# Kernel optimization log

Hardware: AMD Instinct MI355X
Metric: run time of the kernel (lower is better)

The kernel has to match this reference:

```python
import jax, jax.numpy as jnp
import numpy as np
from jax import lax

B, T, D_IN, D_CB, K_CB, H_MID = 32, 512, 1024, 256, 8192, 512

def setup_inputs() -> dict:
    key = jax.random.key(0)
    ks = jax.random.split(key, 12)
    s = 0.02
    return {
        "x": jax.random.normal(ks[0], (B, T, D_IN), jnp.float32),
        "w1": jax.random.normal(ks[1], (H_MID, D_IN), jnp.float32) * s,
        "b1": jnp.zeros((H_MID,), jnp.float32),
        "w2": jax.random.normal(ks[2], (D_CB, H_MID), jnp.float32) * s,
        "b2": jnp.zeros((D_CB,), jnp.float32),
        "conv_w": jax.random.normal(ks[3], (D_CB, D_CB, 3), jnp.float32) * s,
        "conv_b": jnp.zeros((D_CB,), jnp.float32),
        "codebook": jax.random.uniform(ks[4], (K_CB, D_CB), jnp.float32, -1.0 / K_CB, 1.0 / K_CB),
        "gru_wih": jax.random.normal(ks[5], (3 * D_CB, D_CB), jnp.float32) * s,
        "gru_whh": jax.random.normal(ks[6], (3 * D_CB, D_CB), jnp.float32) * s,
        "gru_bih": jnp.zeros((3 * D_CB,), jnp.float32),
        "gru_bhh": jnp.zeros((3 * D_CB,), jnp.float32),
    }

def _forward(x, w1, b1, w2, b2, conv_w, conv_b, codebook, gru_wih, gru_whh, gru_bih, gru_bhh):
    # feature_processor (dropout is identity at eval): [B,T,D_IN] -> [B,T,D_CB]
    h = jax.nn.relu(jnp.einsum('btd,hd->bth', x, w1) + b1)
    h = jax.nn.relu(jnp.einsum('bth,ch->btc', h, w2) + b2)
    # temporal conv1d, kernel 3, pad 1 (T > 1 here)
    f = jnp.transpose(h, (0, 2, 1))  # NCT
    f = lax.conv_general_dilated(f, conv_w, (1,), 'SAME', dimension_numbers=('NCH', 'OIH', 'NCH'))
    f = f + conv_b[None, :, None]
    features = jnp.transpose(f, (0, 2, 1))  # [B,T,D_CB]
    # quantize: squared-Euclidean nearest codebook entry (same argmin as cdist)
    flat = features.reshape(-1, features.shape[-1])  # [B*T, D_CB]
    d2 = (jnp.sum(flat * flat, axis=1, keepdims=True)
          - 2.0 * (flat @ codebook.T)
          + jnp.sum(codebook * codebook, axis=1))  # [B*T, K]
    idx = jnp.argmin(d2, axis=-1)
    quantized = codebook[idx].reshape(features.shape)  # [B,T,D_CB]
    token_indices = idx.reshape(features.shape[0], features.shape[1])
    commitment_loss = jnp.mean((features - lax.stop_gradient(quantized)) ** 2)
    codebook_loss = jnp.mean((quantized - lax.stop_gradient(features)) ** 2)
    # context predictor: 1-layer GRU over quantized[:, :-1]
    q_in = quantized[:, :-1]  # [B,T-1,D_CB]
    xproj = jnp.einsum('btd,hd->bth', q_in, gru_wih) + gru_bih  # [B,T-1,3H]
    Hd = quantized.shape[-1]
    def step(hprev, xt):
        gh = hprev @ gru_whh.T + gru_bhh  # [B,3H]
        xr, xz, xn = xt[:, :Hd], xt[:, Hd:2 * Hd], xt[:, 2 * Hd:]
        hr, hz, hn = gh[:, :Hd], gh[:, Hd:2 * Hd], gh[:, 2 * Hd:]
        r = jax.nn.sigmoid(xr + hr)
        z = jax.nn.sigmoid(xz + hz)
        n = jnp.tanh(xn + r * hn)
        hnew = (1.0 - z) * n + z * hprev
        return hnew, hnew
    h0 = jnp.zeros((q_in.shape[0], Hd), q_in.dtype)
    _, hs = lax.scan(step, h0, jnp.transpose(xproj, (1, 0, 2)))
    context = jnp.transpose(hs, (1, 0, 2))  # [B,T-1,D_CB]
    context_loss = jnp.mean((context - features[:, 1:]) ** 2)
    vq_loss = commitment_loss + 0.25 * codebook_loss + 0.1 * context_loss
    return token_indices, quantized, commitment_loss, codebook_loss, context_loss, vq_loss

def reference(x, w1, b1, w2, b2, conv_w, conv_b, codebook, gru_wih, gru_whh, gru_bih, gru_bhh):
    return _forward(x, w1, b1, w2, b2, conv_w, conv_b, codebook, gru_wih, gru_whh, gru_bih, gru_bhh)
```

## Files before the change

### kernel.cpp

```cpp
#include <hip/hip_runtime.h>
#include <math.h>

#define NB 32
#define NT 512
#define NDIN 1024
#define NDCB 256
#define NKCB 8192
#define NHMID 512
#define NROWS (NB*NT)

typedef _Float16 half2_t __attribute__((ext_vector_type(2)));
typedef _Float16 f16x8 __attribute__((ext_vector_type(8)));
typedef __attribute__((ext_vector_type(8))) short bf16x8;
typedef __attribute__((ext_vector_type(8))) unsigned short u16x8;
typedef __attribute__((ext_vector_type(4))) float f32x4;

__device__ __forceinline__ unsigned short f2bf(float x) {
    unsigned int u = __float_as_uint(x);
    return (unsigned short)((u + 0x7fffu + ((u >> 16) & 1u)) >> 16);
}

#if __has_builtin(__builtin_amdgcn_fdot2)
__device__ __forceinline__ float dot2f(half2_t a, half2_t b, float c) {
    return __builtin_amdgcn_fdot2(a, b, c, false);
}
#else
__device__ __forceinline__ float dot2f(half2_t a, half2_t b, float c) {
    return fmaf((float)a[0], (float)b[0], fmaf((float)a[1], (float)b[1], c));
}
#endif

template<bool RELU>
__global__ __launch_bounds__(256) void gemm_nt_f64_kernel(
    const float* __restrict__ A, const float* __restrict__ Bm,
    const float* __restrict__ bias, float* __restrict__ C,
    int M, int N, int K)
{
    __shared__ double a_s[16*64];
    __shared__ double b_s[16*64];
    const int tid = threadIdx.x;
    const int bn0 = blockIdx.x * 64;
    const int bm0 = blockIdx.y * 64;
    const int lr = tid >> 2;
    const int kq = (tid & 3) << 2;
    const int tx = tid & 15, ty = tid >> 4;
    double acc[4][4] = {};
    const float* Ap = A + (size_t)(bm0 + lr) * K + kq;
    const float* Bp = Bm + (size_t)(bn0 + lr) * K + kq;
    for (int kt = 0; kt < K; kt += 16) {
        float4 a = *(const float4*)(Ap + kt);
        float4 b = *(const float4*)(Bp + kt);
        __syncthreads();
        a_s[(kq+0)*64+lr] = (double)a.x; a_s[(kq+1)*64+lr] = (double)a.y;
        a_s[(kq+2)*64+lr] = (double)a.z; a_s[(kq+3)*64+lr] = (double)a.w;
        b_s[(kq+0)*64+lr] = (double)b.x; b_s[(kq+1)*64+lr] = (double)b.y;
        b_s[(kq+2)*64+lr] = (double)b.z; b_s[(kq+3)*64+lr] = (double)b.w;
        __syncthreads();
        #pragma unroll
        for (int kk = 0; kk < 16; kk++) {
            double aa[4], bb[4];
            #pragma unroll
            for (int u = 0; u < 4; u++) { aa[u] = a_s[kk*64 + ty*4 + u]; bb[u] = b_s[kk*64 + tx*4 + u]; }
            #pragma unroll
            for (int i = 0; i < 4; i++)
                #pragma unroll
                for (int j = 0; j < 4; j++)
                    acc[i][j] = fma(aa[i], bb[j], acc[i][j]);
        }
    }
    const float4 b4 = *(const float4*)&bias[bn0 + tx*4];
    const double bc[4] = {(double)b4.x, (double)b4.y, (double)b4.z, (double)b4.w};
    #pragma unroll
    for (int i = 0; i < 4; i++) {
        float o[4];
        #pragma unroll
        for (int j = 0; j < 4; j++) {
            double v = acc[i][j] + bc[j];
            if (RELU) v = fmax(v, 0.0);
            o[j] = (float)v;
        }
        *(float4*)&C[(size_t)(bm0 + ty*4 + i)*N + bn0 + tx*4] =
            make_float4(o[0], o[1], o[2], o[3]);
    }
}

__global__ __launch_bounds__(256) void conv3_f64_kernel(
    const float* __restrict__ H2, const float* __restrict__ W3,
    const float* __restrict__ bias, float* __restrict__ F)
{
    __shared__ double a_s[16*68];
    __shared__ double b_s[3][16*64];
    const int tid = threadIdx.x;
    const int bn0 = blockIdx.x * 64;
    const int bm0 = blockIdx.y * 64;
    const int lr = tid >> 2;
    const int kq = (tid & 3) << 2;
    const int tx = tid & 15, ty = tid >> 4;
    const int tmod = bm0 & (NT-1);
    const bool has_top = (tmod != 0);
    const bool has_bot = (tmod + 64 < NT);
    double acc[4][4] = {};
    for (int kt = 0; kt < NDCB; kt += 16) {
        float4 a = make_float4(0.f,0.f,0.f,0.f);
        if (lr >= 1 || has_top)
            a = *(const float4*)&H2[(size_t)(bm0 - 1 + lr)*NDCB + kt + kq];
        float4 e = make_float4(0.f,0.f,0.f,0.f);
        int l2 = 0, kq2 = 0;
        if (tid < 8) {
            l2 = 64 + (tid >> 2); kq2 = (tid & 3) << 2;
            if (l2 == 64 || has_bot)
                e = *(const float4*)&H2[(size_t)(bm0 - 1 + l2)*NDCB + kt + kq2];
        }
        float4 w[3];
        #pragma unroll
        for (int s = 0; s < 3; s++)
            w[s] = *(const float4*)&W3[(size_t)s*65536 + (size_t)(bn0 + lr)*NDCB + kt + kq];
        __syncthreads();
        a_s[(kq+0)*68+lr]=(double)a.x; a_s[(kq+1)*68+lr]=(double)a.y;
        a_s[(kq+2)*68+lr]=(double)a.z; a_s[(kq+3)*68+lr]=(double)a.w;
        if (tid < 8) {
            a_s[(kq2+0)*68+l2]=(double)e.x; a_s[(kq2+1)*68+l2]=(double)e.y;
            a_s[(kq2+2)*68+l2]=(double)e.z; a_s[(kq2+3)*68+l2]=(double)e.w;
        }
        #pragma unroll
        for (int s = 0; s < 3; s++) {
            b_s[s][(kq+0)*64+lr]=(double)w[s].x; b_s[s][(kq+1)*64+lr]=(double)w[s].y;
            b_s[s][(kq+2)*64+lr]=(double)w[s].z; b_s[s][(kq+3)*64+lr]=(double)w[s].w;
        }
        __syncthreads();
        #pragma unroll
        for (int kk = 0; kk < 16; kk++) {
            double aa[6];
            #pragma unroll
            for (int u = 0; u < 6; u++) aa[u] = a_s[kk*68 + ty*4 + u];
            #pragma unroll
            for (int s = 0; s < 3; s++) {
                double bb[4];
                #pragma unroll
                for (int u = 0; u < 4; u++) bb[u] = b_s[s][kk*64 + tx*4 + u];
                #pragma unroll
                for (int i = 0; i < 4; i++)
                    #pragma unroll
                    for (int j = 0; j < 4; j++)
                        acc[i][j] = fma(aa[i+s], bb[j], acc[i][j]);
            }
        }
    }
    const float4 b4 = *(const float4*)&bias[bn0 + tx*4];
    const double bc[4] = {(double)b4.x, (double)b4.y, (double)b4.z, (double)b4.w};
    #pragma unroll
    for (int i = 0; i < 4; i++) {
        const size_t base = (size_t)(bm0 + ty*4 + i)*NDCB + bn0 + tx*4;
        *(float4*)&F[base] = make_float4((float)(acc[i][0]+bc[0]), (float)(acc[i][1]+bc[1]),
                                         (float)(acc[i][2]+bc[2]), (float)(acc[i][3]+bc[3]));
    }
}

__global__ __launch_bounds__(512) void vq_kernel(
    const float* __restrict__ F, const float* __restrict__ CB,
    const unsigned short* __restrict__ CBH,
    const float* __restrict__ cnorm, float* __restrict__ idx_out,
    float* __restrict__ qout, float* __restrict__ msd_acc)
{
    __shared__ unsigned short a_bf[64*256];
    __shared__ unsigned short b_bf[128*256];
    __shared__ float cn_s[128];
    __shared__ float red_v[64*64];
    __shared__ int   red_i[64*64];
    __shared__ int   bests[64];
    __shared__ int   cand[64][12];
    __shared__ int   ccnt[64];
    const int tid = threadIdx.x;
    const int m0 = blockIdx.x * 64;

    #pragma unroll
    for (int u = 0; u < 4; u++) {
        int e = tid + u*512;
        int row = e >> 5, c = e & 31;
        const float* src = &F[(size_t)(m0+row)*NDCB + c*8];
        float4 f0 = *(const float4*)src;
        float4 f1 = *(const float4*)(src+4);
        u16x8 p;
        p[0]=f2bf(f0.x); p[1]=f2bf(f0.y); p[2]=f2bf(f0.z); p[3]=f2bf(f0.w);
        p[4]=f2bf(f1.x); p[5]=f2bf(f1.y); p[6]=f2bf(f1.z); p[7]=f2bf(f1.w);
        *(u16x8*)((char*)a_bf + row*512 + ((c*16) ^ ((row&7)<<4))) = p;
    }

    const int w = tid >> 6, lane = tid & 63;
    const int l15 = lane & 15, kg = lane >> 4;
    const int rbase = (w & 3) << 4, cbase = (w >> 2) << 6;
    const char* aP = (const char*)a_bf + (size_t)(rbase + l15)*512;
    const char* bP = (const char*)b_bf + (size_t)(cbase + l15)*512;
    const int swz = (lane & 7) << 4;

    float mv1[4], mv2[4]; int mi1[4], mi2[4];
    #pragma unroll
    for (int i = 0; i < 4; i++) { mv1[i]=3.0e38f; mv2[i]=3.0e38f; mi1[i]=0x7fffffff; mi2[i]=0x7fffffff; }

    for (int n0 = 0; n0 < NKCB; n0 += 128) {
        __syncthreads();
        #pragma unroll
        for (int u = 0; u < 8; u++) {
            int e = tid + u*512;
            int row = e >> 5, c = e & 31;
            u16x8 v = *(const u16x8*)&CBH[(size_t)(n0+row)*NDCB + c*8];
            *(u16x8*)((char*)b_bf + row*512 + ((c*16) ^ ((row&7)<<4))) = v;
        }
        if (tid < 128) cn_s[tid] = cnorm[n0 + tid];
        __syncthreads();
        f32x4 acc[4] = {{0.f,0.f,0.f,0.f},{0.f,0.f,0.f,0.f},{0.f,0.f,0.f,0.f},{0.f,0.f,0.f,0.f}};
        #pragma unroll
        for (int kt = 0; kt < 8; kt++) {
            const int ko = (kt*64 + kg*16) ^ swz;
            bf16x8 av = *(const bf16x8*)(aP + ko);
            #pragma unroll
            for (int f = 0; f < 4; f++) {
                bf16x8 bv = *(const bf16x8*)(bP + f*8192 + ko);
                acc[f] = __builtin_amdgcn_mfma_f32_16x16x32_bf16(av, bv, acc[f], 0, 0, 0);
            }
        }
        #pragma unroll
        for (int f = 0; f < 4; f++) {
            const int col = n0 + cbase + f*16 + l15;
            const float cnv = cn_s[cbase + f*16 + l15];
            #pragma unroll
            for (int i = 0; i < 4; i++) {
                float s = fmaf(-2.0f, acc[f][i], cnv);
                if (s < mv1[i]) { mv2[i]=mv1[i]; mi2[i]=mi1[i]; mv1[i]=s; mi1[i]=col; }
                else if (s < mv2[i]) { mv2[i]=s; mi2[i]=col; }
            }
        }
    }
    #pragma unroll
    for (int i = 0; i < 4; i++) {
        const int row = rbase + kg*4 + i;
        const int eb  = (w>>2)*32 + l15*2;
        red_v[row*64 + eb]   = mv1[i]; red_i[row*64 + eb]   = mi1[i];
        red_v[row*64 + eb+1] = mv2[i]; red_i[row*64 + eb+1] = mi2[i];
    }
    __syncthreads();
    if (tid < 64) {
        float bv = 3.0e38f; int bi = 0x7fffffff;
        for (int e = 0; e < 64; e++) {
            float v = red_v[tid*64 + e]; int ii = red_i[tid*64 + e];
            if (v < bv || (v == bv && ii < bi)) { bv = v; bi = ii; }
        }
        int cnt = 0;
        for (int e = 0; e < 64; e++) {
            if (red_v[tid*64 + e] < bv + 1.0e-5f) {
                if (cnt < 12) cand[tid][cnt] = red_i[tid*64 + e];
                cnt++;
            }
        }
        bests[tid] = bi;
        ccnt[tid] = (cnt > 12) ? 12 : cnt;
    }
    __syncthreads();
    {
        const int wid = tid >> 6, lane2 = tid & 63;
        for (int r = wid; r < 64; r += 8) {
            const int nc = ccnt[r];
            if (nc < 2) continue;
            double sf = 0.0;
            #pragma unroll
            for (int u = 0; u < 4; u++) {
                double fv = (double)F[(size_t)(m0+r)*NDCB + lane2*4 + u];
                sf = fma(fv, fv, sf);
            }
            #pragma unroll
            for (int off = 32; off > 0; off >>= 1) sf += __shfl_down(sf, off);
            const float sf32 = (float)sf;
            float bd2 = 0.0f; int bidx = 0x7fffffff;
            for (int c = 0; c < nc; c++) {
                const int k = cand[r][c];
                double g = 0.0;
                #pragma unroll
                for (int u = 0; u < 4; u++) {
                    double cv = (double)CB[(size_t)k*NDCB + lane2*4 + u];
                    double fv = (double)F[(size_t)(m0+r)*NDCB + lane2*4 + u];
                    g = fma(cv, fv, g);
                }
                #pragma unroll
                for (int off = 32; off > 0; off >>= 1) g += __shfl_down(g, off);
                if (lane2 == 0) {
                    const float G32 = (float)g;
                    const float t  = sf32 - 2.0f*G32;
                    const float d2 = t + cnorm[k];
                    if (c == 0 || d2 < bd2 || (d2 == bd2 && k < bidx)) { bd2 = d2; bidx = k; }
                }
            }
            if (lane2 == 0) bests[r] = bidx;
        }
    }
    __syncthreads();
    if (tid < 64) idx_out[m0 + tid] = (float)bests[tid];
    float lsum = 0.0f;
    #pragma unroll
    for (int s = 0; s < 8; s++) {
        int e = tid + s*512;
        int row = e >> 6, kqe = (e & 63) << 2;
        float4 q = *(const float4*)&CB[(size_t)bests[row]*NDCB + kqe];
        float4 f = *(const float4*)&F[(size_t)(m0+row)*NDCB + kqe];
        float dx=f.x-q.x, dy=f.y-q.y, dz=f.z-q.z, dw=f.w-q.w;
        lsum += dx*dx + dy*dy + dz*dz + dw*dw;
        *(float4*)&qout[(size_t)(m0+row)*NDCB + kqe] = q;
    }
    red_v[tid] = lsum;
    __syncthreads();
    for (int off = 256; off > 0; off >>= 1) {
        if (tid < off) red_v[tid] += red_v[tid + off];
        __syncthreads();
    }
    if (tid == 0) atomicAdd(msd_acc, red_v[0]);
}

__global__ __launch_bounds__(512) void xproj_mfma_kernel(
    const float* __restrict__ Q, const unsigned short* __restrict__ WIHH,
    const float* __restrict__ bias, float* __restrict__ C)
{
    __shared__ unsigned short a_h[64*256];
    __shared__ unsigned short b_h[128*256];
    const int tid = threadIdx.x;
    const int m0 = blockIdx.x * 64;

    #pragma unroll
    for (int u = 0; u < 4; u++) {
        int e = tid + u*512;
        int row = e >> 5, c = e & 31;
        const float* src = &Q[(size_t)(m0+row)*NDCB + c*8];
        float4 f0 = *(const float4*)src;
        float4 f1 = *(const float4*)(src+4);
        f16x8 p;
        p[0]=(_Float16)(f0.x*8192.0f); p[1]=(_Float16)(f0.y*8192.0f);
        p[2]=(_Float16)(f0.z*8192.0f); p[3]=(_Float16)(f0.w*8192.0f);
        p[4]=(_Float16)(f1.x*8192.0f); p[5]=(_Float16)(f1.y*8192.0f);
        p[6]=(_Float16)(f1.z*8192.0f); p[7]=(_Float16)(f1.w*8192.0f);
        *(f16x8*)((char*)a_h + row*512 + ((c*16) ^ ((row&7)<<4))) = p;
    }

    const int w = tid >> 6, lane = tid & 63;
    const int l15 = lane & 15, kg = lane >> 4;
    const int rbase = (w & 3) << 4, cbase = (w >> 2) << 6;
    const char* aP = (const char*)a_h + (size_t)(rbase + l15)*512;
    const char* bP = (const char*)b_h + (size_t)(cbase + l15)*512;
    const int swz = (lane & 7) << 4;

    for (int n0 = 0; n0 < 768; n0 += 128) {
        __syncthreads();
        #pragma unroll
        for (int u = 0; u < 8; u++) {
            int e = tid + u*512;
            int row = e >> 5, c = e & 31;
            u16x8 v = *(const u16x8*)&WIHH[(size_t)(n0+row)*NDCB + c*8];
            *(u16x8*)((char*)b_h + row*512 + ((c*16) ^ ((row&7)<<4))) = v;
        }
        __syncthreads();
        f32x4 acc[4] = {{0.f,0.f,0.f,0.f},{0.f,0.f,0.f,0.f},{0.f,0.f,0.f,0.f},{0.f,0.f,0.f,0.f}};
        #pragma unroll
        for (int kt = 0; kt < 8; kt++) {
            const int ko = (kt*64 + kg*16) ^ swz;
            f16x8 av = *(const f16x8*)(aP + ko);
            #pragma unroll
            for (int f = 0; f < 4; f++) {
                f16x8 bv = *(const f16x8*)(bP + f*8192 + ko);
                acc[f] = __builtin_amdgcn_mfma_f32_16x16x32_f16(av, bv, acc[f], 0, 0, 0);
            }
        }
        #pragma unroll
        for (int f = 0; f < 4; f++) {
            const int col = n0 + cbase + f*16 + l15;
            const float bv = bias[col];
            #pragma unroll
            for (int i = 0; i < 4; i++) {
                const int row = m0 + rbase + kg*4 + i;
                C[(size_t)row*768 + col] = fmaf(acc[f][i], 1.0f/8192.0f, bv);
            }
        }
    }
}

__device__ __forceinline__ void gru_body(
    const float* __restrict__ XP, const float* __restrict__ WHH,
    const float* __restrict__ bhh, const float* __restrict__ F,
    float* __restrict__ ctx_acc)
{
    __shared__ float part[3][2][256];
    __shared__ uint4 hpk[2][32];
    __shared__ float red[256];
    const int tid = threadIdx.x;
    const int b = blockIdx.x;
    const int j = tid & 255;
    const int q = tid >> 8;
    half2_t wr[64], wz[64], wn[64];
    {
        const float* rp = WHH + (size_t)j*256 + q*128;
        #pragma unroll
        for (int k = 0; k < 32; k++) {
            float4 vr = *(const float4*)(rp + 4*k);
            float4 vz = *(const float4*)(rp + 65536 + 4*k);
            float4 vn = *(const float4*)(rp + 131072 + 4*k);
            wr[2*k+0] = (half2_t){(_Float16)vr.x, (_Float16)vr.y};
            wr[2*k+1] = (half2_t){(_Float16)vr.z, (_Float16)vr.w};
            wz[2*k+0] = (half2_t){(_Float16)vz.x, (_Float16)vz.y};
            wz[2*k+1] = (half2_t){(_Float16)vz.z, (_Float16)vz.w};
            wn[2*k+0] = (half2_t){(_Float16)vn.x, (_Float16)vn.y};
            wn[2*k+1] = (half2_t){(_Float16)vn.z, (_Float16)vn.w};
        }
    }
    if (tid < 64) hpk[tid >> 5][tid & 31] = make_uint4(0u, 0u, 0u, 0u);
    const float bb0 = bhh[j], bb1 = bhh[256+j], bb2 = bhh[512+j];
    const float* xpb = XP + (size_t)b*NT*768;
    const float* fb  = F  + (size_t)b*NT*NDCB;
    float hprev = 0.0f, lsum = 0.0f;
    __syncthreads();
    int cur = 0;
    for (int t = 0; t < NT-1; t++) {
        float xr = 0.f, xz = 0.f, xn = 0.f, fv = 0.f;
        if (tid < 256) {
            const float* xp = xpb + (size_t)t*768;
            xr = xp[j]; xz = xp[256+j]; xn = xp[512+j];
            fv = fb[(size_t)(t+1)*NDCB + j];
        }
        float a0=0.f, c0=0.f, a1=0.f, c1=0.f, a2=0.f, c2=0.f;
        #pragma unroll
        for (int kk = 0; kk < 16; kk++) {
            uint4 hp = hpk[cur][q*16 + kk];
            half2_t h0 = __builtin_bit_cast(half2_t, hp.x);
            half2_t h1 = __builtin_bit_cast(half2_t, hp.y);
            half2_t h2 = __builtin_bit_cast(half2_t, hp.z);
            half2_t h3 = __builtin_bit_cast(half2_t, hp.w);
            a0 = dot2f(wr[4*kk+0], h0, a0); c0 = dot2f(wr[4*kk+1], h1, c0);
            a1 = dot2f(wz[4*kk+0], h0, a1); c1 = dot2f(wz[4*kk+1], h1, c1);
            a2 = dot2f(wn[4*kk+0], h0, a2); c2 = dot2f(wn[4*kk+1], h1, c2);
            a0 = dot2f(wr[4*kk+2], h2, a0); c0 = dot2f(wr[4*kk+3], h3, c0);
            a1 = dot2f(wz[4*kk+2], h2, a1); c1 = dot2f(wz[4*kk+3], h3, c1);
            a2 = dot2f(wn[4*kk+2], h2, a2); c2 = dot2f(wn[4*kk+3], h3, c2);
        }
        part[0][q][j] = a0 + c0; part[1][q][j] = a1 + c1; part[2][q][j] = a2 + c2;
        __syncthreads();
        if (tid < 256) {
            float ghr = part[0][0][j] + part[0][1][j] + bb0;
            float ghz = part[1][0][j] + part[1][1][j] + bb1;
            float ghn = part[2][0][j] + part[2][1][j] + bb2;
            float r = 1.0f/(1.0f + __expf(-(xr + ghr)));
            float z = 1.0f/(1.0f + __expf(-(xz + ghz)));
            float v = fmaf(r, ghn, xn);
            v = fminf(fmaxf(v, -12.0f), 12.0f);
            float ev = __expf(-2.0f*v);
            float n = (1.0f - ev)/(1.0f + ev);
            float hnew = (1.0f - z)*n + z*hprev;
            float d = hnew - fv;
            lsum = fmaf(d, d, lsum);
            float nb = __shfl_down(hnew, 1);
            if (!(j & 1)) {
                half2_t p; p[0] = (_Float16)hnew; p[1] = (_Float16)nb;
                ((unsigned int*)&hpk[cur ^ 1][0])[j >> 1] = __builtin_bit_cast(unsigned int, p);
            }
            hprev = hnew;
        }
        __syncthreads();
        cur ^= 1;
    }
    if (tid < 256) red[j] = lsum;
    __syncthreads();
    for (int off = 128; off > 0; off >>= 1) {
        if (tid < off) red[tid] += red[tid + off];
        __syncthreads();
    }
    if (tid == 0) atomicAdd(ctx_acc, red[0]);
}

__global__ __attribute__((amdgpu_flat_work_group_size(512, 512), amdgpu_waves_per_eu(2, 2)))
void gru_a(const float* __restrict__ XP, const float* __restrict__ WHH,
           const float* __restrict__ bhh, const float* __restrict__ F,
           float* __restrict__ ctx_acc)
{ gru_body(XP, WHH, bhh, F, ctx_acc); }

__global__ __launch_bounds__(512, 2)
void gru_b(const float* __restrict__ XP, const float* __restrict__ WHH,
           const float* __restrict__ bhh, const float* __restrict__ F,
           float* __restrict__ ctx_acc)
{ gru_body(XP, WHH, bhh, F, ctx_acc); }

__global__ __launch_bounds__(512)
void gru_c(const float* __restrict__ XP, const float* __restrict__ WHH,
           const float* __restrict__ bhh, const float* __restrict__ F,
           float* __restrict__ ctx_acc)
{ gru_body(XP, WHH, bhh, F, ctx_acc); }

__global__ __launch_bounds__(256) void prep_kernel(
    const float* __restrict__ conv_w, float* __restrict__ w3,
    const float* __restrict__ wih, unsigned short* __restrict__ wihh,
    float* __restrict__ accv)
{
    int e = blockIdx.x*256 + threadIdx.x;
    if (e == 0) { accv[0] = 0.0f; accv[1] = 0.0f; }
    {
        int k = e >> 16;
        int r = e & 65535;
        int c = r >> 8, i = r & 255;
        w3[e] = conv_w[(size_t)c*768 + i*3 + k];
    }
    {
        _Float16 h = (_Float16)wih[e];
        wihh[e] = __builtin_bit_cast(unsigned short, h);
    }
}

__global__ __launch_bounds__(256) void cb2bf_kernel(
    const float* __restrict__ cb, unsigned short* __restrict__ cbh)
{
    int e = (blockIdx.x*256 + threadIdx.x) * 4;
    float4 v = *(const float4*)&cb[e];
    unsigned short p0 = f2bf(v.x), p1 = f2bf(v.y), p2 = f2bf(v.z), p3 = f2bf(v.w);
    unsigned long long pk = (unsigned long long)p0 | ((unsigned long long)p1 << 16)
                          | ((unsigned long long)p2 << 32) | ((unsigned long long)p3 << 48);
    *(unsigned long long*)&cbh[e] = pk;
}

__global__ __launch_bounds__(64) void cnorm_kernel(
    const float* __restrict__ CB, float* __restrict__ cn)
{
    const int k = blockIdx.x;
    const int lane = threadIdx.x;
    float4 v = *(const float4*)&CB[(size_t)k*NDCB + lane*4];
    double s = (double)v.x*(double)v.x + (double)v.y*(double)v.y
             + (double)v.z*(double)v.z + (double)v.w*(double)v.w;
    #pragma unroll
    for (int off = 32; off > 0; off >>= 1) s += __shfl_down(s, off);
    if (lane == 0) cn[k] = (float)s;
}

__global__ void finalize_kernel(const float* __restrict__ acc, float* __restrict__ out)
{
    if (threadIdx.x == 0) {
        float msd = acc[0] * (1.0f/4194304.0f);
        float ctx = acc[1] * (1.0f/4184064.0f);
        out[0] = msd;
        out[1] = msd;
        out[2] = ctx;
        out[3] = 1.25f*msd + 0.1f*ctx;
    }
}

extern "C" void kernel_launch(void* const* d_in, const int* in_sizes, int n_in,
                              void* d_out, int out_size, void* d_ws, size_t ws_size,
                              hipStream_t stream) {
    const float* x      = (const float*)d_in[0];
    const float* w1     = (const float*)d_in[1];
    const float* b1     = (const float*)d_in[2];
    const float* w2     = (const float*)d_in[3];
    const float* b2     = (const float*)d_in[4];
    const float* conv_w = (const float*)d_in[5];
    const float* conv_b = (const float*)d_in[6];
    const float* cb     = (const float*)d_in[7];
    const float* wih    = (const float*)d_in[8];
    const float* whh    = (const float*)d_in[9];
    const float* bih    = (const float*)d_in[10];
    const float* bhh    = (const float*)d_in[11];
    float* out = (float*)d_out;

    char* ws = (char*)d_ws;
    float*  feat   = (float*)(ws + 0);
    float*  h1     = (float*)(ws + 16777216);
    float*  xproj  = (float*)(ws + 16777216);
    float*  h2     = (float*)(ws + 50331648);
    unsigned short* cbh = (unsigned short*)(ws + 50331648);
    float*  cn     = (float*)(ws + 67108864);
    float*  w3     = (float*)(ws + 67141632);
    unsigned short* wihh = (unsigned short*)(ws + 67928064);
    float*  accv   = (float*)(ws + 68714496);

    float* idx_out = out;
    float* qout    = out + 16384;
    float* louts   = out + 16384 + 4194304;

    static int gsel = -1;
    if (gsel < 0) {
        hipFuncAttributes fa;
        gsel = 2;
        if (hipFuncGetAttributes(&fa, reinterpret_cast<const void*>(gru_a)) == hipSuccess
            && fa.localSizeBytes == 0 && fa.numRegs >= 193) gsel = 0;
        else if (hipFuncGetAttributes(&fa, reinterpret_cast<const void*>(gru_b)) == hipSuccess
            && fa.localSizeBytes == 0 && fa.numRegs >= 193) gsel = 1;
    }

    prep_kernel<<<768, 256, 0, stream>>>(conv_w, w3, wih, wihh, accv);
    cnorm_kernel<<<NKCB, 64, 0, stream>>>(cb, cn);
    gemm_nt_f64_kernel<true ><<<dim3(NHMID/64, NROWS/64), 256, 0, stream>>>(x,  w1, b1, h1, NROWS, NHMID, NDIN);
    gemm_nt_f64_kernel<true ><<<dim3(NDCB/64,  NROWS/64), 256, 0, stream>>>(h1, w2, b2, h2, NROWS, NDCB, NHMID);
    conv3_f64_kernel<<<dim3(NDCB/64, NROWS/64), 256, 0, stream>>>(h2, w3, conv_b, feat);
    cb2bf_kernel<<<2048, 256, 0, stream>>>(cb, cbh);
    vq_kernel<<<NROWS/64, 512, 0, stream>>>(feat, cb, cbh, cn, idx_out, qout, accv);
    xproj_mfma_kernel<<<NROWS/64, 512, 0, stream>>>(qout, wihh, bih, xproj);
    if (gsel == 0)      gru_a<<<NB, 512, 0, stream>>>(xproj, whh, bhh, feat, accv + 1);
    else if (gsel == 1) gru_b<<<NB, 512, 0, stream>>>(xproj, whh, bhh, feat, accv + 1);
    else                gru_c<<<NB, 512, 0, stream>>>(xproj, whh, bhh, feat, accv + 1);
    finalize_kernel<<<1, 64, 0, stream>>>(accv, louts);
}
```

Measured before the change: 1.780 ms.

## Split GRU recurrent matvec across 1024 threads per batch block

Adds a GRU kernel variant where each batch block uses 1024 threads, with four threads per hidden unit each holding a quarter of the W_hh row in registers. This halves the per-thread serial dot-product chain and the register footprint on every recurrent step. In exchange, the partial-sum reduction across shared memory grows from two to four slices per gate. A host-side attribute probe picks the first variant that keeps its weights in registers without spilling, otherwise it falls back to the old 512-thread kernel.

```diff
diff --git a/kernel.cpp b/kernel.cpp
--- a/kernel.cpp
+++ b/kernel.cpp
@@ -379,10 +379,119 @@
     }
 }
 
-__device__ __forceinline__ void gru_body(
+__device__ __forceinline__ void gru_body_1024(
     const float* __restrict__ XP, const float* __restrict__ WHH,
     const float* __restrict__ bhh, const float* __restrict__ F,
     float* __restrict__ ctx_acc)
+{
+    __shared__ float part[3][4][256];
+    __shared__ uint4 hpk[2][32];
+    __shared__ float red[256];
+    const int tid = threadIdx.x;
+    const int b = blockIdx.x;
+    const int j = tid & 255;
+    const int q = tid >> 8;
+    half2_t wr[32], wz[32], wn[32];
+    {
+        const float* rp = WHH + (size_t)j*256 + q*64;
+        #pragma unroll
+        for (int k = 0; k < 16; k++) {
+            float4 vr = *(const float4*)(rp + 4*k);
+            float4 vz = *(const float4*)(rp + 65536 + 4*k);
+            float4 vn = *(const float4*)(rp + 131072 + 4*k);
+            wr[2*k+0] = (half2_t){(_Float16)vr.x, (_Float16)vr.y};
+            wr[2*k+1] = (half2_t){(_Float16)vr.z, (_Float16)vr.w};
+            wz[2*k+0] = (half2_t){(_Float16)vz.x, (_Float16)vz.y};
+            wz[2*k+1] = (half2_t){(_Float16)vz.z, (_Float16)vz.w};
+            wn[2*k+0] = (half2_t){(_Float16)vn.x, (_Float16)vn.y};
+            wn[2*k+1] = (half2_t){(_Float16)vn.z, (_Float16)vn.w};
+        }
+    }
+    if (tid < 64) hpk[tid >> 5][tid & 31] = make_uint4(0u, 0u, 0u, 0u);
+    const float bb0 = bhh[j], bb1 = bhh[256+j], bb2 = bhh[512+j];
+    const float* xpb = XP + (size_t)b*NT*768;
+    const float* fb  = F  + (size_t)b*NT*NDCB;
+    float hprev = 0.0f, lsum = 0.0f;
+    __syncthreads();
+    int cur = 0;
+    for (int t = 0; t < NT-1; t++) {
+        float xr = 0.f, xz = 0.f, xn = 0.f, fv = 0.f;
+        if (tid < 256) {
+            const float* xp = xpb + (size_t)t*768;
+            xr = xp[j]; xz = xp[256+j]; xn = xp[512+j];
+            fv = fb[(size_t)(t+1)*NDCB + j];
+        }
+        float a0=0.f, c0=0.f, a1=0.f, c1=0.f, a2=0.f, c2=0.f;
+        #pragma unroll
+        for (int kk = 0; kk < 8; kk++) {
+            uint4 hp = hpk[cur][q*8 + kk];
+            half2_t h0 = __builtin_bit_cast(half2_t, hp.x);
+            half2_t h1 = __builtin_bit_cast(half2_t, hp.y);
+            half2_t h2 = __builtin_bit_cast(half2_t, hp.z);
+            half2_t h3 = __builtin_bit_cast(half2_t, hp.w);
+            a0 = dot2f(wr[4*kk+0], h0, a0); c0 = dot2f(wr[4*kk+1], h1, c0);
+            a1 = dot2f(wz[4*kk+0], h0, a1); c1 = dot2f(wz[4*kk+1], h1, c1);
+            a2 = dot2f(wn[4*kk+0], h0, a2); c2 = dot2f(wn[4*kk+1], h1, c2);
+            a0 = dot2f(wr[4*kk+2], h2, a0); c0 = dot2f(wr[4*kk+3], h3, c0);
+            a1 = dot2f(wz[4*kk+2], h2, a1); c1 = dot2f(wz[4*kk+3], h3, c1);
+            a2 = dot2f(wn[4*kk+2], h2, a2); c2 = dot2f(wn[4*kk+3], h3, c2);
+        }
+        part[0][q][j] = a0 + c0; part[1][q][j] = a1 + c1; part[2][q][j] = a2 + c2;
+        __syncthreads();
+        if (tid < 256) {
+            float ghr = part[0][0][j] + part[0][1][j] + part[0][2][j] + part[0][3][j] + bb0;
+            float ghz = part[1][0][j] + part[1][1][j] + part[1][2][j] + part[1][3][j] + bb1;
+            float ghn = part[2][0][j] + part[2][1][j] + part[2][2][j] + part[2][3][j] + bb2;
+            float r = 1.0f/(1.0f + __expf(-(xr + ghr)));
+            float z = 1.0f/(1.0f + __expf(-(xz + ghz)));
+            float v = fmaf(r, ghn, xn);
+            v = fminf(fmaxf(v, -12.0f), 12.0f);
+            float ev = __expf(-2.0f*v);
+            float n = (1.0f - ev)/(1.0f + ev);
+            float hnew = (1.0f - z)*n + z*hprev;
+            float d = hnew - fv;
+            lsum = fmaf(d, d, lsum);
+            float nb = __shfl_down(hnew, 1);
+            if (!(j & 1)) {
+                half2_t p; p[0] = (_Float16)hnew; p[1] = (_Float16)nb;
+                ((unsigned int*)&hpk[cur ^ 1][0])[j >> 1] = __builtin_bit_cast(unsigned int, p);
+            }
+            hprev = hnew;
+        }
+        __syncthreads();
+        cur ^= 1;
+    }
+    if (tid < 256) red[j] = lsum;
+    __syncthreads();
+    for (int off = 128; off > 0; off >>= 1) {
+        if (tid < off) red[tid] += red[tid + off];
+        __syncthreads();
+    }
+    if (tid == 0) atomicAdd(ctx_acc, red[0]);
+}
+
+__global__ __launch_bounds__(1024, 1)
+void gru_w1(const float* __restrict__ XP, const float* __restrict__ WHH,
+            const float* __restrict__ bhh, const float* __restrict__ F,
+            float* __restrict__ ctx_acc)
+{ gru_body_1024(XP, WHH, bhh, F, ctx_acc); }
+
+__global__ __launch_bounds__(1024, 4)
+void gru_w2(const float* __restrict__ XP, const float* __restrict__ WHH,
+            const float* __restrict__ bhh, const float* __restrict__ F,
+            float* __restrict__ ctx_acc)
+{ gru_body_1024(XP, WHH, bhh, F, ctx_acc); }
+
+__global__ __attribute__((amdgpu_flat_work_group_size(1024, 1024), amdgpu_waves_per_eu(4, 4)))
+void gru_w3(const float* __restrict__ XP, const float* __restrict__ WHH,
+            const float* __restrict__ bhh, const float* __restrict__ F,
+            float* __restrict__ ctx_acc)
+{ gru_body_1024(XP, WHH, bhh, F, ctx_acc); }
+
+__global__ __launch_bounds__(512)
+void gru_c(const float* __restrict__ XP, const float* __restrict__ WHH,
+           const float* __restrict__ bhh, const float* __restrict__ F,
+           float* __restrict__ ctx_acc)
 {
     __shared__ float part[3][2][256];
     __shared__ uint4 hpk[2][32];
@@ -470,24 +579,6 @@
     if (tid == 0) atomicAdd(ctx_acc, red[0]);
 }
 
-__global__ __attribute__((amdgpu_flat_work_group_size(512, 512), amdgpu_waves_per_eu(2, 2)))
-void gru_a(const float* __restrict__ XP, const float* __restrict__ WHH,
-           const float* __restrict__ bhh, const float* __restrict__ F,
-           float* __restrict__ ctx_acc)
-{ gru_body(XP, WHH, bhh, F, ctx_acc); }
-
-__global__ __launch_bounds__(512, 2)
-void gru_b(const float* __restrict__ XP, const float* __restrict__ WHH,
-           const float* __restrict__ bhh, const float* __restrict__ F,
-           float* __restrict__ ctx_acc)
-{ gru_body(XP, WHH, bhh, F, ctx_acc); }
-
-__global__ __launch_bounds__(512)
-void gru_c(const float* __restrict__ XP, const float* __restrict__ WHH,
-           const float* __restrict__ bhh, const float* __restrict__ F,
-           float* __restrict__ ctx_acc)
-{ gru_body(XP, WHH, bhh, F, ctx_acc); }
-
 __global__ __launch_bounds__(256) void prep_kernel(
     const float* __restrict__ conv_w, float* __restrict__ w3,
     const float* __restrict__ wih, unsigned short* __restrict__ wihh,
@@ -577,12 +668,19 @@
 
     static int gsel = -1;
     if (gsel < 0) {
-        hipFuncAttributes fa;
-        gsel = 2;
-        if (hipFuncGetAttributes(&fa, reinterpret_cast<const void*>(gru_a)) == hipSuccess
-            && fa.localSizeBytes == 0 && fa.numRegs >= 193) gsel = 0;
-        else if (hipFuncGetAttributes(&fa, reinterpret_cast<const void*>(gru_b)) == hipSuccess
-            && fa.localSizeBytes == 0 && fa.numRegs >= 193) gsel = 1;
+        const void* cands[3] = {
+            reinterpret_cast<const void*>(gru_w1),
+            reinterpret_cast<const void*>(gru_w2),
+            reinterpret_cast<const void*>(gru_w3) };
+        gsel = 3;
+        for (int pass = 0; pass < 2 && gsel == 3; ++pass) {
+            size_t lim = (pass == 0) ? 0 : 64;
+            for (int i = 0; i < 3 && gsel == 3; ++i) {
+                hipFuncAttributes fa;
+                if (hipFuncGetAttributes(&fa, cands[i]) == hipSuccess
+                    && fa.localSizeBytes <= lim && fa.numRegs >= 116) gsel = i;
+            }
+        }
     }
 
     prep_kernel<<<768, 256, 0, stream>>>(conv_w, w3, wih, wihh, accv);
@@ -593,8 +691,9 @@
     cb2bf_kernel<<<2048, 256, 0, stream>>>(cb, cbh);
     vq_kernel<<<NROWS/64, 512, 0, stream>>>(feat, cb, cbh, cn, idx_out, qout, accv);
     xproj_mfma_kernel<<<NROWS/64, 512, 0, stream>>>(qout, wihh, bih, xproj);
-    if (gsel == 0)      gru_a<<<NB, 512, 0, stream>>>(xproj, whh, bhh, feat, accv + 1);
-    else if (gsel == 1) gru_b<<<NB, 512, 0, stream>>>(xproj, whh, bhh, feat, accv + 1);
+    if (gsel == 0)      gru_w1<<<NB, 1024, 0, stream>>>(xproj, whh, bhh, feat, accv + 1);
+    else if (gsel == 1) gru_w2<<<NB, 1024, 0, stream>>>(xproj, whh, bhh, feat, accv + 1);
+    else if (gsel == 2) gru_w3<<<NB, 1024, 0, stream>>>(xproj, whh, bhh, feat, accv + 1);
     else                gru_c<<<NB, 512, 0, stream>>>(xproj, whh, bhh, feat, accv + 1);
     finalize_kernel<<<1, 64, 0, stream>>>(accv, louts);
 }
```

Result: no change. 1.762 ms (-1.0%).
